# Optimization experiments

Hardware: AMD Instinct MI355X
Metric: run time of the kernel (lower is better)

## Reference

```python
import jax, jax.numpy as jnp
import numpy as np

N_TYPES = 7
DT = 0.1
TAU_INIT = 20.0


def setup_inputs() -> dict:
    key = jax.random.key(0)
    k0, k1, k2, k3 = jax.random.split(key, 4)
    N = 49000          # n_neurons, divisible by 7 types
    E = 1_600_000      # n_edges (~avg degree 32)
    B = 8              # batch (via explicit v_init)
    n_tm1 = N // N_TYPES
    type_ids = (jnp.arange(N) % N_TYPES).astype(jnp.int32)   # type 0 == 'Tm1'
    tm1_indices = jnp.arange(0, N, N_TYPES, dtype=jnp.int32)  # positions where type_ids==0
    return {
        "tm1_input": jax.random.normal(k0, (B, n_tm1), jnp.float32),
        "v_init": jnp.zeros((B, N), jnp.float32),
        "weights": jax.random.normal(k1, (E,), jnp.float32),
        "bias": jnp.zeros((N,), jnp.float32),
        "tau_params": jnp.full((N_TYPES,), TAU_INIT, jnp.float32),
        "scale_excitatory": jnp.ones((), jnp.float32),
        "scale_inhibitory": jnp.ones((), jnp.float32),
        "source_indices": jax.random.randint(k2, (E,), 0, N, dtype=jnp.int32),
        "target_indices": jax.random.randint(k3, (E,), 0, N, dtype=jnp.int32),
        "type_ids": type_ids,
        "tm1_indices": tm1_indices,
        "steps": 100,
    }


def reference(tm1_input, v_init, weights, bias, tau_params,
              scale_excitatory, scale_inhibitory,
              source_indices, target_indices, type_ids, tm1_indices, steps):
    # per-neuron tau from per-type params (torch: get_tau_vector via masks)
    tau = tau_params[type_ids]                                   # [N]
    one = jnp.ones((), weights.dtype)
    edge_scales = jnp.where(weights > 0, scale_excitatory,
                            jnp.where(weights < 0, scale_inhibitory, one))
    scaled_weights = weights * edge_scales                       # [E]

    def step(v, _):
        v = v.at[:, tm1_indices].set(tm1_input)                  # clamp Tm1 neurons
        r = jax.nn.relu(v)                                       # activation
        edge_currents = r[:, source_indices] * scaled_weights    # gather [B,E]
        syn = jnp.zeros_like(v).at[:, target_indices].add(edge_currents)  # scatter-add [B,N]
        dv = (-v + syn + bias) / tau
        dv = dv.at[:, tm1_indices].set(0.0)                      # Tm1 held fixed
        return v + DT * dv, None

    v, _ = jax.lax.scan(step, v_init, None, length=steps)
    return v
```

## Files before the change

### kernel.cpp

```cpp
#include <hip/hip_runtime.h>


#define BLK 256
#define STEPS 100
#define NBATCH 8
#define PRE 5
static constexpr float DT_C = 0.1f;

typedef unsigned uv4 __attribute__((ext_vector_type(4)));

__device__ __forceinline__ unsigned f2bf_rne(float x) {
    unsigned u = __float_as_uint(x);
    return (u + 0x7FFFu + ((u >> 16) & 1u)) >> 16;
}
__device__ __forceinline__ unsigned pk_bf2(float a, float b) {
    return f2bf_rne(a) | (f2bf_rne(b) << 16);
}

__global__ void k_zero(int* counts, int* countS, int* tm1_pos, int N) {
    int i = blockIdx.x * BLK + threadIdx.x;
    if (i < N) { counts[i] = 0; countS[i] = 0; tm1_pos[i] = -1; }
}

__global__ void k_tm1pos(const int* __restrict__ tm1_idx, int* tm1_pos, int NT) {
    int i = blockIdx.x * BLK + threadIdx.x;
    if (i < NT) tm1_pos[tm1_idx[i]] = i;
}

__global__ void k_hist(const int* __restrict__ srcI, const int* __restrict__ tgt,
                       const int* __restrict__ type_ids,
                       int* counts, int* countS, unsigned char* __restrict__ flagA,
                       int E) {
    int i = blockIdx.x * BLK + threadIdx.x;
    if (i >= E) return;
    int t = tgt[i];
    atomicAdd(&counts[t], 1);
    unsigned char st = (type_ids[srcI[i]] == 0) ? 1 : 0;
    if (st) atomicAdd(&countS[t], 1);
    flagA[i] = st;
}

__global__ void k_scan1(const int* __restrict__ counts, int* offsets, int* bsum, int N) {
    __shared__ int s[BLK];
    int tx = threadIdx.x;
    int i = blockIdx.x * BLK + tx;
    int v = (i < N) ? counts[i] : 0;
    s[tx] = v; __syncthreads();
    for (int d = 1; d < BLK; d <<= 1) {
        int t = (tx >= d) ? s[tx - d] : 0;
        __syncthreads();
        s[tx] += t;
        __syncthreads();
    }
    if (i < N) offsets[i] = s[tx] - v;
    if (tx == BLK - 1) bsum[blockIdx.x] = s[tx];
}

__global__ void k_scan2(int* bsum, int nb) {
    __shared__ int s[BLK];
    int tx = threadIdx.x;
    int v = (tx < nb) ? bsum[tx] : 0;
    s[tx] = v; __syncthreads();
    for (int d = 1; d < BLK; d <<= 1) {
        int t = (tx >= d) ? s[tx - d] : 0;
        __syncthreads();
        s[tx] += t;
        __syncthreads();
    }
    if (tx < nb) bsum[tx] = s[tx] - v;
}

__global__ void k_scan3c(const int* __restrict__ bsum, const int* __restrict__ countS,
                         int* offsets, int* cursorD, int* cursorS, int* dynEnd,
                         int N, int E) {
    int i = blockIdx.x * BLK + threadIdx.x;
    if (i > N) return;
    if (i == N) { offsets[N] = E; return; }
    int o = offsets[i] + bsum[i >> 8];
    offsets[i] = o;
}

__global__ void k_cursors(const int* __restrict__ offsets, const int* __restrict__ countS,
                          int* cursorD, int* cursorS, int* dynEnd, int N) {
    int i = blockIdx.x * BLK + threadIdx.x;
    if (i >= N) return;
    int o  = offsets[i];
    int dE = offsets[i + 1] - countS[i];
    cursorD[i] = o;
    cursorS[i] = dE;
    dynEnd[i]  = dE;
}

__global__ void k_fill(const int* __restrict__ srcI, const int* __restrict__ tgtI,
                       const float* __restrict__ w,
                       const float* __restrict__ se, const float* __restrict__ si,
                       const unsigned char* __restrict__ flagA,
                       int* cursorD, int* cursorS, unsigned* __restrict__ csr, int E) {
    int i = blockIdx.x * BLK + threadIdx.x;
    if (i >= E) return;
    float wv = w[i];
    float sc = wv > 0.f ? se[0] : (wv < 0.f ? si[0] : 1.f);
    float sw = wv * sc;
    unsigned entry = (f2bf_rne(sw) << 16) | (unsigned)srcI[i];
    int t = tgtI[i];
    int pos = flagA[i] ? atomicAdd(&cursorS[t], 1) : atomicAdd(&cursorD[t], 1);
    csr[pos] = entry;
}

__global__ void k_initv(const float* __restrict__ tm1_in, const float* __restrict__ v_init,
                        const float* __restrict__ tau_p,
                        const int* __restrict__ type_ids, const int* __restrict__ tm1_pos,
                        float* __restrict__ v_w, uint4* __restrict__ r0, uint4* __restrict__ r1,
                        float2* __restrict__ coef2, int N, int NT) {
    int n = blockIdx.x * BLK + threadIdx.x;
    if (n >= N) return;
    int k = tm1_pos[n];
    float g = DT_C / tau_p[type_ids[n]];
    coef2[n] = make_float2((k >= 0) ? 0.f : (1.f - g), g);
    float vv[NBATCH], rr[NBATCH];
    for (int b = 0; b < NBATCH; ++b) {
        float val = (k >= 0) ? tm1_in[b * NT + k] : v_init[b * N + n];
        vv[b] = val;
        rr[b] = fmaxf(val, 0.f);
    }
    float4* vp = (float4*)(v_w + (size_t)n * 8);
    vp[0] = make_float4(vv[0], vv[1], vv[2], vv[3]);
    vp[1] = make_float4(vv[4], vv[5], vv[6], vv[7]);
    uint4 rq = make_uint4(pk_bf2(rr[0], rr[1]), pk_bf2(rr[2], rr[3]),
                          pk_bf2(rr[4], rr[5]), pk_bf2(rr[6], rr[7]));
    r0[n] = rq;
    r1[n] = rq;
}

__device__ __forceinline__ float butterfly8(float4 a0, float4 a1, int sub) {
    int bit0 = sub & 1, bit1 = (sub >> 1) & 1, bit2 = (sub >> 2) & 1;
    float b0 = (bit0 ? a0.y : a0.x) + __shfl_xor(bit0 ? a0.x : a0.y, 1);
    float b1 = (bit0 ? a0.w : a0.z) + __shfl_xor(bit0 ? a0.z : a0.w, 1);
    float b2 = (bit0 ? a1.y : a1.x) + __shfl_xor(bit0 ? a1.x : a1.y, 1);
    float b3 = (bit0 ? a1.w : a1.z) + __shfl_xor(bit0 ? a1.z : a1.w, 1);
    float c0 = (bit1 ? b1 : b0) + __shfl_xor(bit1 ? b0 : b1, 2);
    float c1 = (bit1 ? b3 : b2) + __shfl_xor(bit1 ? b2 : b3, 2);
    return (bit2 ? c1 : c0) + __shfl_xor(bit2 ? c0 : c1, 4);
}

__global__ void k_static(const int* __restrict__ offsets, const int* __restrict__ dynEnd,
                         const unsigned* __restrict__ csr, const uint4* __restrict__ r0,
                         const float2* __restrict__ coef2, const float* __restrict__ bias,
                         float* __restrict__ cF, int N) {
    int tid = blockIdx.x * BLK + threadIdx.x;
    int n = tid >> 3;
    int sub = threadIdx.x & 7;
    if (n >= N) return;
    float g = coef2[n].y;
    int s = dynEnd[n], e = offsets[n + 1];
    float4 a0 = make_float4(0.f, 0.f, 0.f, 0.f);
    float4 a1 = make_float4(0.f, 0.f, 0.f, 0.f);
    for (int i = s + sub; i < e; i += 8) {
        unsigned ew = csr[i];
        float w = __uint_as_float(ew & 0xFFFF0000u);
        uint4 q = r0[ew & 0xFFFFu];
        a0.x = fmaf(w, __uint_as_float(q.x << 16),          a0.x);
        a0.y = fmaf(w, __uint_as_float(q.x & 0xFFFF0000u),  a0.y);
        a0.z = fmaf(w, __uint_as_float(q.y << 16),          a0.z);
        a0.w = fmaf(w, __uint_as_float(q.y & 0xFFFF0000u),  a0.w);
        a1.x = fmaf(w, __uint_as_float(q.z << 16),          a1.x);
        a1.y = fmaf(w, __uint_as_float(q.z & 0xFFFF0000u),  a1.y);
        a1.z = fmaf(w, __uint_as_float(q.w << 16),          a1.z);
        a1.w = fmaf(w, __uint_as_float(q.w & 0xFFFF0000u),  a1.w);
    }
    float syn = butterfly8(a0, a1, sub);
    cF[(size_t)n * 8 + sub] = (syn + bias[n]) * g;
}

__global__ __launch_bounds__(BLK) void k_step(
        const int* __restrict__ offsets, const int* __restrict__ dynEnd,
        const unsigned* __restrict__ csr,
        const float2* __restrict__ coef2, const float* __restrict__ cF,
        const uv4* __restrict__ r_prev,
        float* __restrict__ v_w, unsigned short* __restrict__ r_next, int N) {
    int tid = blockIdx.x * BLK + threadIdx.x;
    int n = tid >> 3;
    int sub = threadIdx.x & 7;
    if (n >= N) return;
    float2 cf = coef2[n];
    if (cf.x == 0.f) return;
    int s = offsets[n], e = dynEnd[n];

    float wj[PRE];
    int   sj[PRE];
    #pragma unroll
    for (int j = 0; j < PRE; ++j) {
        int idx = s + sub + 8 * j;
        unsigned ew = (idx < e) ? __builtin_nontemporal_load(csr + idx) : 0u;
        wj[j] = __uint_as_float(ew & 0xFFFF0000u);
        sj[j] = (int)(ew & 0xFFFFu);
    }
    uv4 q[PRE];
    #pragma unroll
    for (int j = 0; j < PRE; ++j) {
        int idx = s + sub + 8 * j;
        q[j] = (idx < e) ? r_prev[sj[j]] : (uv4)(0u);
    }
    float4 a0 = make_float4(0.f, 0.f, 0.f, 0.f);
    float4 a1 = make_float4(0.f, 0.f, 0.f, 0.f);
    #pragma unroll
    for (int j = 0; j < PRE; ++j) {
        float w = wj[j];
        a0.x = fmaf(w, __uint_as_float(q[j].x << 16),          a0.x);
        a0.y = fmaf(w, __uint_as_float(q[j].x & 0xFFFF0000u),  a0.y);
        a0.z = fmaf(w, __uint_as_float(q[j].y << 16),          a0.z);
        a0.w = fmaf(w, __uint_as_float(q[j].y & 0xFFFF0000u),  a0.w);
        a1.x = fmaf(w, __uint_as_float(q[j].z << 16),          a1.x);
        a1.y = fmaf(w, __uint_as_float(q[j].z & 0xFFFF0000u),  a1.y);
        a1.z = fmaf(w, __uint_as_float(q[j].w << 16),          a1.z);
        a1.w = fmaf(w, __uint_as_float(q[j].w & 0xFFFF0000u),  a1.w);
    }
    for (int i = s + sub + 8 * PRE; i < e; i += 8) {
        unsigned ew = __builtin_nontemporal_load(csr + i);
        float w = __uint_as_float(ew & 0xFFFF0000u);
        uv4 qq = r_prev[ew & 0xFFFFu];
        a0.x = fmaf(w, __uint_as_float(qq.x << 16),          a0.x);
        a0.y = fmaf(w, __uint_as_float(qq.x & 0xFFFF0000u),  a0.y);
        a0.z = fmaf(w, __uint_as_float(qq.y << 16),          a0.z);
        a0.w = fmaf(w, __uint_as_float(qq.y & 0xFFFF0000u),  a0.w);
        a1.x = fmaf(w, __uint_as_float(qq.z << 16),          a1.x);
        a1.y = fmaf(w, __uint_as_float(qq.z & 0xFFFF0000u),  a1.y);
        a1.z = fmaf(w, __uint_as_float(qq.w << 16),          a1.z);
        a1.w = fmaf(w, __uint_as_float(qq.w & 0xFFFF0000u),  a1.w);
    }
    float syn = butterfly8(a0, a1, sub);
    size_t idx = (size_t)n * 8 + sub;
    float vo = __builtin_nontemporal_load(v_w + idx);
    float cf3 = __builtin_nontemporal_load(cF + idx);
    float vn = vo * cf.x + syn * cf.y + cf3;
    __builtin_nontemporal_store(vn, v_w + idx);
    r_next[idx] = (unsigned short)f2bf_rne(fmaxf(vn, 0.f));
}

__global__ void k_out(const float* __restrict__ v_w, float* __restrict__ out, int N) {
    int t = blockIdx.x * BLK + threadIdx.x;
    if (t >= NBATCH * N) return;
    int b = t / N;
    int n = t - b * N;
    out[t] = v_w[(size_t)n * 8 + b];
}

static inline size_t align16(size_t x) { return (x + 15) & ~(size_t)15; }

extern "C" void kernel_launch(void* const* d_in, const int* in_sizes, int n_in,
                              void* d_out, int out_size, void* d_ws, size_t ws_size,
                              hipStream_t stream) {
    const float* tm1_in  = (const float*)d_in[0];
    const float* v_init  = (const float*)d_in[1];
    const float* weights = (const float*)d_in[2];
    const float* bias    = (const float*)d_in[3];
    const float* tau_p   = (const float*)d_in[4];
    const float* se      = (const float*)d_in[5];
    const float* si      = (const float*)d_in[6];
    const int*   srcI    = (const int*)d_in[7];
    const int*   tgtI    = (const int*)d_in[8];
    const int*   type_ids= (const int*)d_in[9];
    const int*   tm1_idx = (const int*)d_in[10];

    const int E  = in_sizes[2];
    const int N  = in_sizes[3];
    const int NT = in_sizes[10];

    char* p = (char*)d_ws;
    size_t off = 0;
    auto take = [&](size_t bytes) { void* r = p + off; off += align16(bytes); return r; };
    int*      offsets = (int*)     take((size_t)(N + 1) * 4);
    int*      cursorD = (int*)     take((size_t)N * 4);
    int*      cursorS = (int*)     take((size_t)N * 4);
    int*      counts  = (int*)     take((size_t)N * 4);
    int*      countS  = (int*)     take((size_t)N * 4);
    int*      dynEnd  = (int*)     take((size_t)N * 4);
    int*      tm1_pos = (int*)     take((size_t)N * 4);
    int*      bsum    = (int*)     take(1024 * 4);
    unsigned char* flagA = (unsigned char*)take((size_t)E);
    unsigned* csr     = (unsigned*)take((size_t)E * 4);
    float2*   coef2   = (float2*)  take((size_t)N * 8);
    float*    cF      = (float*)   take((size_t)N * 8 * 4);
    float*    v_w     = (float*)   take((size_t)N * 8 * 4);
    uint4*    r0      = (uint4*)   take((size_t)N * 16);
    uint4*    r1      = (uint4*)   take((size_t)N * 16);
    (void)ws_size;

    const int gN  = (N + BLK - 1) / BLK;
    const int gN1 = (N + 1 + BLK - 1) / BLK;
    const int gE  = (E + BLK - 1) / BLK;
    const int gNT = (NT + BLK - 1) / BLK;
    const int g8  = (N * 8 + BLK - 1) / BLK;

    k_zero<<<gN, BLK, 0, stream>>>(counts, countS, tm1_pos, N);
    k_tm1pos<<<gNT, BLK, 0, stream>>>(tm1_idx, tm1_pos, NT);
    k_hist<<<gE, BLK, 0, stream>>>(srcI, tgtI, type_ids, counts, countS, flagA, E);
    k_scan1<<<gN, BLK, 0, stream>>>(counts, offsets, bsum, N);
    k_scan2<<<1, BLK, 0, stream>>>(bsum, gN);
    k_scan3c<<<gN1, BLK, 0, stream>>>(bsum, countS, offsets, cursorD, cursorS,
                                      dynEnd, N, E);
    k_cursors<<<gN, BLK, 0, stream>>>(offsets, countS, cursorD, cursorS, dynEnd, N);
    k_fill<<<gE, BLK, 0, stream>>>(srcI, tgtI, weights, se, si, flagA,
                                   cursorD, cursorS, csr, E);
    k_initv<<<gN, BLK, 0, stream>>>(tm1_in, v_init, tau_p, type_ids, tm1_pos,
                                    v_w, r0, r1, coef2, N, NT);
    k_static<<<g8, BLK, 0, stream>>>(offsets, dynEnd, csr, r0, coef2, bias, cF, N);

    uint4* rb[2] = { r0, r1 };
    for (int s = 0; s < STEPS; ++s) {
        k_step<<<g8, BLK, 0, stream>>>(offsets, dynEnd, csr, coef2, cF,
                                       (const uv4*)rb[s & 1], v_w,
                                       (unsigned short*)rb[(s + 1) & 1], N);
    }
    k_out<<<g8, BLK, 0, stream>>>(v_w, (float*)d_out, N);
}
```

Before: 1.234 ms.

## Build CSR via two-pass bucketed placement and fuse output write into last step

Replaces the global-atomic CSR fill with a two-level bucket sort. Each block first groups its edges by target range in LDS and writes them contiguously to a temporary 64-bit buffer. A second kernel then places the edges within each range using LDS atomics. The final step writes the transposed output directly, which removes the separate output kernel, and the prefetch depth rises from 5 to 6. The intent is to reduce scattered global atomics and writes during setup, at the cost of an extra 8-byte-per-edge temporary buffer and an additional pass over it.

```diff
diff --git a/kernel.cpp b/kernel.cpp
--- a/kernel.cpp
+++ b/kernel.cpp
@@ -4,7 +4,10 @@
 #define BLK 256
 #define STEPS 100
 #define NBATCH 8
-#define PRE 5
+#define PRE 6
+#define NBUCK 256
+#define CHUNK 4096
+#define PERT 16
 static constexpr float DT_C = 0.1f;
 
 typedef unsigned uv4 __attribute__((ext_vector_type(4)));
@@ -70,41 +73,111 @@
     if (tx < nb) bsum[tx] = s[tx] - v;
 }
 
-__global__ void k_scan3c(const int* __restrict__ bsum, const int* __restrict__ countS,
-                         int* offsets, int* cursorD, int* cursorS, int* dynEnd,
-                         int N, int E) {
-    int i = blockIdx.x * BLK + threadIdx.x;
-    if (i > N) return;
-    if (i == N) { offsets[N] = E; return; }
-    int o = offsets[i] + bsum[i >> 8];
-    offsets[i] = o;
-}
-
-__global__ void k_cursors(const int* __restrict__ offsets, const int* __restrict__ countS,
-                          int* cursorD, int* cursorS, int* dynEnd, int N) {
-    int i = blockIdx.x * BLK + threadIdx.x;
-    if (i >= N) return;
-    int o  = offsets[i];
-    int dE = offsets[i + 1] - countS[i];
-    cursorD[i] = o;
-    cursorS[i] = dE;
-    dynEnd[i]  = dE;
-}
-
-__global__ void k_fill(const int* __restrict__ srcI, const int* __restrict__ tgtI,
-                       const float* __restrict__ w,
-                       const float* __restrict__ se, const float* __restrict__ si,
-                       const unsigned char* __restrict__ flagA,
-                       int* cursorD, int* cursorS, unsigned* __restrict__ csr, int E) {
-    int i = blockIdx.x * BLK + threadIdx.x;
-    if (i >= E) return;
-    float wv = w[i];
-    float sc = wv > 0.f ? se[0] : (wv < 0.f ? si[0] : 1.f);
-    float sw = wv * sc;
-    unsigned entry = (f2bf_rne(sw) << 16) | (unsigned)srcI[i];
-    int t = tgtI[i];
-    int pos = flagA[i] ? atomicAdd(&cursorS[t], 1) : atomicAdd(&cursorD[t], 1);
-    csr[pos] = entry;
+__global__ void k_scan3(const int* __restrict__ bsum, int* offsets, int N, int E) {
+    int i = blockIdx.x * BLK + threadIdx.x;
+    if (i < N) offsets[i] += bsum[i >> 8];
+    else if (i == N) offsets[N] = E;
+}
+
+__global__ void k_prep(const int* __restrict__ offsets, const int* __restrict__ countS,
+                       int* dynEnd, int* gCursor, int N, int span) {
+    int i = blockIdx.x * BLK + threadIdx.x;
+    if (i < N) dynEnd[i] = offsets[i + 1] - countS[i];
+    if (i < NBUCK) {
+        int t0 = i * span; if (t0 > N) t0 = N;
+        gCursor[i] = offsets[t0];
+    }
+}
+
+__global__ __launch_bounds__(256) void k_bucket(
+        const int* __restrict__ srcI, const int* __restrict__ tgtI,
+        const float* __restrict__ w,
+        const float* __restrict__ se, const float* __restrict__ si,
+        const unsigned char* __restrict__ flagA,
+        int* gCursor, unsigned long long* __restrict__ csr_tmp, int E, int span) {
+    __shared__ unsigned long long stg[CHUNK];
+    __shared__ int hcnt[NBUCK], hcur[NBUCK], hbase[NBUCK], gb[NBUCK], sc1[NBUCK];
+    int base = blockIdx.x * CHUNK;
+    int cnt = E - base; if (cnt > CHUNK) cnt = CHUNK;
+    int tx = threadIdx.x;
+    hcnt[tx] = 0;
+    __syncthreads();
+
+    float sE = se[0], sI = si[0];
+    unsigned long long ent[PERT];
+    int ebk[PERT];
+    #pragma unroll
+    for (int k = 0; k < PERT; ++k) {
+        int o = k * 256 + tx;
+        ent[k] = 0; ebk[k] = -1;
+        if (o < cnt) {
+            int i = base + o;
+            int t = tgtI[i], s = srcI[i];
+            float wv = w[i];
+            float sc = wv > 0.f ? sE : (wv < 0.f ? sI : 1.f);
+            unsigned wb = f2bf_rne(wv * sc);
+            unsigned long long fl = flagA[i] ? (1ull << 63) : 0ull;
+            ent[k] = (unsigned long long)(unsigned)t
+                   | ((unsigned long long)(unsigned)s << 16)
+                   | ((unsigned long long)wb << 32) | fl;
+            int b = t / span;
+            ebk[k] = b;
+            atomicAdd(&hcnt[b], 1);
+        }
+    }
+    __syncthreads();
+    int v = hcnt[tx];
+    sc1[tx] = v; __syncthreads();
+    for (int d = 1; d < NBUCK; d <<= 1) {
+        int t2 = (tx >= d) ? sc1[tx - d] : 0;
+        __syncthreads();
+        sc1[tx] += t2;
+        __syncthreads();
+    }
+    hbase[tx] = sc1[tx] - v;
+    hcur[tx]  = sc1[tx] - v;
+    gb[tx] = atomicAdd(&gCursor[tx], v);
+    __syncthreads();
+    #pragma unroll
+    for (int k = 0; k < PERT; ++k) {
+        if (ebk[k] >= 0) {
+            int r = atomicAdd(&hcur[ebk[k]], 1);
+            stg[r] = ent[k];
+        }
+    }
+    __syncthreads();
+    for (int idx = tx; idx < cnt; idx += 256) {
+        unsigned long long e = stg[idx];
+        int b = (int)(e & 0xFFFFu) / span;
+        csr_tmp[gb[b] + (idx - hbase[b])] = e;
+    }
+}
+
+__global__ __launch_bounds__(256) void k_place(
+        const int* __restrict__ offsets, const int* __restrict__ dynEnd,
+        const unsigned long long* __restrict__ csr_tmp,
+        unsigned* __restrict__ csr, int N, int span) {
+    __shared__ int curD[256], curS[256];
+    int b = blockIdx.x;
+    int n0 = b * span;
+    int nE = n0 + span; if (nE > N) nE = N;
+    if (n0 >= N) return;
+    int tx = threadIdx.x;
+    for (int l = tx; l < nE - n0; l += 256) {
+        curD[l] = offsets[n0 + l];
+        curS[l] = dynEnd[n0 + l];
+    }
+    __syncthreads();
+    int s = offsets[n0], e = offsets[nE];
+    for (int i = s + tx; i < e; i += 256) {
+        unsigned long long en = csr_tmp[i];
+        int t = (int)(en & 0xFFFFu);
+        int l = t - n0;
+        int pos = (en >> 63) ? atomicAdd(&curS[l], 1) : atomicAdd(&curD[l], 1);
+        unsigned src = (unsigned)((en >> 16) & 0xFFFFu);
+        unsigned wb  = (unsigned)((en >> 32) & 0xFFFFu);
+        csr[pos] = (wb << 16) | src;
+    }
 }
 
 __global__ void k_initv(const float* __restrict__ tm1_in, const float* __restrict__ v_init,
@@ -177,29 +250,34 @@
         const unsigned* __restrict__ csr,
         const float2* __restrict__ coef2, const float* __restrict__ cF,
         const uv4* __restrict__ r_prev,
-        float* __restrict__ v_w, unsigned short* __restrict__ r_next, int N) {
+        float* __restrict__ v_w, unsigned short* __restrict__ r_next,
+        float* __restrict__ out, int N) {
     int tid = blockIdx.x * BLK + threadIdx.x;
     int n = tid >> 3;
     int sub = threadIdx.x & 7;
     if (n >= N) return;
     float2 cf = coef2[n];
-    if (cf.x == 0.f) return;
+    size_t idx = (size_t)n * 8 + sub;
+    if (cf.x == 0.f) {
+        if (out) out[(size_t)sub * N + n] = v_w[idx];
+        return;
+    }
     int s = offsets[n], e = dynEnd[n];
 
     float wj[PRE];
     int   sj[PRE];
     #pragma unroll
     for (int j = 0; j < PRE; ++j) {
-        int idx = s + sub + 8 * j;
-        unsigned ew = (idx < e) ? __builtin_nontemporal_load(csr + idx) : 0u;
+        int i2 = s + sub + 8 * j;
+        unsigned ew = (i2 < e) ? __builtin_nontemporal_load(csr + i2) : 0u;
         wj[j] = __uint_as_float(ew & 0xFFFF0000u);
         sj[j] = (int)(ew & 0xFFFFu);
     }
     uv4 q[PRE];
     #pragma unroll
     for (int j = 0; j < PRE; ++j) {
-        int idx = s + sub + 8 * j;
-        q[j] = (idx < e) ? r_prev[sj[j]] : (uv4)(0u);
+        int i2 = s + sub + 8 * j;
+        q[j] = (i2 < e) ? r_prev[sj[j]] : (uv4)(0u);
     }
     float4 a0 = make_float4(0.f, 0.f, 0.f, 0.f);
     float4 a1 = make_float4(0.f, 0.f, 0.f, 0.f);
@@ -215,8 +293,8 @@
         a1.z = fmaf(w, __uint_as_float(q[j].w << 16),          a1.z);
         a1.w = fmaf(w, __uint_as_float(q[j].w & 0xFFFF0000u),  a1.w);
     }
-    for (int i = s + sub + 8 * PRE; i < e; i += 8) {
-        unsigned ew = __builtin_nontemporal_load(csr + i);
+    for (int i2 = s + sub + 8 * PRE; i2 < e; i2 += 8) {
+        unsigned ew = __builtin_nontemporal_load(csr + i2);
         float w = __uint_as_float(ew & 0xFFFF0000u);
         uv4 qq = r_prev[ew & 0xFFFFu];
         a0.x = fmaf(w, __uint_as_float(qq.x << 16),          a0.x);
@@ -229,20 +307,15 @@
         a1.w = fmaf(w, __uint_as_float(qq.w & 0xFFFF0000u),  a1.w);
     }
     float syn = butterfly8(a0, a1, sub);
-    size_t idx = (size_t)n * 8 + sub;
     float vo = __builtin_nontemporal_load(v_w + idx);
     float cf3 = __builtin_nontemporal_load(cF + idx);
     float vn = vo * cf.x + syn * cf.y + cf3;
-    __builtin_nontemporal_store(vn, v_w + idx);
-    r_next[idx] = (unsigned short)f2bf_rne(fmaxf(vn, 0.f));
-}
-
-__global__ void k_out(const float* __restrict__ v_w, float* __restrict__ out, int N) {
-    int t = blockIdx.x * BLK + threadIdx.x;
-    if (t >= NBATCH * N) return;
-    int b = t / N;
-    int n = t - b * N;
-    out[t] = v_w[(size_t)n * 8 + b];
+    if (out) {
+        out[(size_t)sub * N + n] = vn;
+    } else {
+        __builtin_nontemporal_store(vn, v_w + idx);
+        r_next[idx] = (unsigned short)f2bf_rne(fmaxf(vn, 0.f));
+    }
 }
 
 static inline size_t align16(size_t x) { return (x + 15) & ~(size_t)15; }
@@ -265,20 +338,21 @@
     const int E  = in_sizes[2];
     const int N  = in_sizes[3];
     const int NT = in_sizes[10];
+    const int span = (N + NBUCK - 1) / NBUCK;
 
     char* p = (char*)d_ws;
     size_t off = 0;
     auto take = [&](size_t bytes) { void* r = p + off; off += align16(bytes); return r; };
     int*      offsets = (int*)     take((size_t)(N + 1) * 4);
-    int*      cursorD = (int*)     take((size_t)N * 4);
-    int*      cursorS = (int*)     take((size_t)N * 4);
     int*      counts  = (int*)     take((size_t)N * 4);
     int*      countS  = (int*)     take((size_t)N * 4);
     int*      dynEnd  = (int*)     take((size_t)N * 4);
     int*      tm1_pos = (int*)     take((size_t)N * 4);
     int*      bsum    = (int*)     take(1024 * 4);
+    int*      gCursor = (int*)     take(NBUCK * 4);
     unsigned char* flagA = (unsigned char*)take((size_t)E);
     unsigned* csr     = (unsigned*)take((size_t)E * 4);
+    unsigned long long* csr_tmp = (unsigned long long*)take((size_t)E * 8);
     float2*   coef2   = (float2*)  take((size_t)N * 8);
     float*    cF      = (float*)   take((size_t)N * 8 * 4);
     float*    v_w     = (float*)   take((size_t)N * 8 * 4);
@@ -291,26 +365,28 @@
     const int gE  = (E + BLK - 1) / BLK;
     const int gNT = (NT + BLK - 1) / BLK;
     const int g8  = (N * 8 + BLK - 1) / BLK;
+    const int gCH = (E + CHUNK - 1) / CHUNK;
 
     k_zero<<<gN, BLK, 0, stream>>>(counts, countS, tm1_pos, N);
     k_tm1pos<<<gNT, BLK, 0, stream>>>(tm1_idx, tm1_pos, NT);
     k_hist<<<gE, BLK, 0, stream>>>(srcI, tgtI, type_ids, counts, countS, flagA, E);
     k_scan1<<<gN, BLK, 0, stream>>>(counts, offsets, bsum, N);
     k_scan2<<<1, BLK, 0, stream>>>(bsum, gN);
-    k_scan3c<<<gN1, BLK, 0, stream>>>(bsum, countS, offsets, cursorD, cursorS,
-                                      dynEnd, N, E);
-    k_cursors<<<gN, BLK, 0, stream>>>(offsets, countS, cursorD, cursorS, dynEnd, N);
-    k_fill<<<gE, BLK, 0, stream>>>(srcI, tgtI, weights, se, si, flagA,
-                                   cursorD, cursorS, csr, E);
+    k_scan3<<<gN1, BLK, 0, stream>>>(bsum, offsets, N, E);
+    k_prep<<<gN, BLK, 0, stream>>>(offsets, countS, dynEnd, gCursor, N, span);
+    k_bucket<<<gCH, 256, 0, stream>>>(srcI, tgtI, weights, se, si, flagA,
+                                      gCursor, csr_tmp, E, span);
+    k_place<<<NBUCK, 256, 0, stream>>>(offsets, dynEnd, csr_tmp, csr, N, span);
     k_initv<<<gN, BLK, 0, stream>>>(tm1_in, v_init, tau_p, type_ids, tm1_pos,
                                     v_w, r0, r1, coef2, N, NT);
     k_static<<<g8, BLK, 0, stream>>>(offsets, dynEnd, csr, r0, coef2, bias, cF, N);
 
     uint4* rb[2] = { r0, r1 };
     for (int s = 0; s < STEPS; ++s) {
+        float* outp = (s == STEPS - 1) ? (float*)d_out : nullptr;
         k_step<<<g8, BLK, 0, stream>>>(offsets, dynEnd, csr, coef2, cF,
                                        (const uv4*)rb[s & 1], v_w,
-                                       (unsigned short*)rb[(s + 1) & 1], N);
-    }
-    k_out<<<g8, BLK, 0, stream>>>(v_w, (float*)d_out, N);
-}
+                                       (unsigned short*)rb[(s + 1) & 1],
+                                       outp, N);
+    }
+}
```

Result: faster. 1.158 ms (-6.2%).
